# Optimization experiments

Hardware: AMD Instinct MI355X
Metric: run time of the kernel (lower is better)

The kernel has to match this reference:

```python
import jax, jax.numpy as jnp
import numpy as np

B, IN, OUT, BR = 64, 8192, 2048, 4
VTH = 0.5
_SQRT_2PI = float(np.sqrt(2.0 * np.pi))


def _gauss(x, mu, sigma):
    return jnp.exp(-((x - mu) ** 2) / (2.0 * sigma ** 2)) / _SQRT_2PI / sigma


@jax.custom_vjp
def act_fun(x):
    return (x > 0.0).astype(x.dtype)


def _act_fwd(x):
    return act_fun(x), x


def _act_bwd(x, g):
    lens, scale, hight, gamma = 0.5, 6.0, 0.15, 0.5
    temp = (_gauss(x, 0.0, lens) * (1.0 + hight)
            - _gauss(x, lens, scale * lens) * hight
            - _gauss(x, -lens, scale * lens) * hight)
    return (g * temp * gamma,)


act_fun.defvjp(_act_fwd, _act_bwd)


def setup_inputs() -> dict:
    key = jax.random.key(0)
    ks = jax.random.split(key, 8)
    fan_in = IN
    bound = 1.0 / np.sqrt(fan_in)
    return {
        "input_spike": jax.random.uniform(ks[0], (B, IN), dtype=jnp.float32),
        "mem": jax.random.uniform(ks[1], (B, OUT), dtype=jnp.float32),
        "spike": jax.random.uniform(ks[2], (B, OUT), dtype=jnp.float32),
        "d_input": jnp.zeros((B, OUT, BR), dtype=jnp.float32),
        "v_th": jnp.ones((B, OUT), dtype=jnp.float32) * VTH,
        "W": jax.random.uniform(ks[3], (OUT * BR, IN), minval=-bound, maxval=bound, dtype=jnp.float32),
        "b": jax.random.uniform(ks[4], (OUT * BR,), minval=-bound, maxval=bound, dtype=jnp.float32),
        "tau_m": jax.random.uniform(ks[5], (OUT,), minval=0.0, maxval=4.0, dtype=jnp.float32),
        "tau_n": jax.random.uniform(ks[6], (OUT, BR), minval=0.0, maxval=4.0, dtype=jnp.float32),
    }


def reference(input_spike, mem, spike, d_input, v_th, W, b, tau_m, tau_n):
    R_m = 1.0
    batch = input_spike.shape[0]
    out_dim, branch = tau_n.shape
    in_dim = W.shape[1]  # padded input size
    chunk = in_dim // branch
    # pad input to in_dim (pad == 0 for these dims, kept for generality)
    pad = in_dim - input_spike.shape[1]
    k = jnp.pad(input_spike.astype(jnp.float32), ((0, 0), (0, pad)))
    # block-masked linear: mask keeps, for neuron o / branch j, only column block j.
    # Equivalent to taking the diagonal blocks of W reshaped [out, branch, branch, chunk].
    W_diag = jnp.einsum("obbc->obc", W.reshape(out_dim, branch, branch, chunk))
    y = jnp.einsum("obc,nbc->nob", W_diag, k.reshape(batch, branch, chunk))
    y = y + b.reshape(out_dim, branch)  # [B, out, branch]
    # per-branch dendritic decay
    beta = jax.nn.sigmoid(tau_n)
    d_new = beta * d_input + (1.0 - beta) * y
    l_input = d_new.sum(axis=2)  # [B, out]
    # LIF with soft reset
    alpha = jax.nn.sigmoid(tau_m)
    mem_new = mem * alpha + (1.0 - alpha) * R_m * l_input - v_th * spike
    spike_new = act_fun(mem_new - v_th)
    return mem_new, spike_new
```

## Files before the change

kernel.cpp:

```cpp
#include <hip/hip_runtime.h>
#include <math.h>

#define BATCH   64
#define IN_DIM  8192
#define OUT_DIM 2048
#define BRANCH  4
#define CHUNK   2048
#define NSEG    2
#define KSEG    1024
#define KT      128
#define NT      8

typedef __attribute__((ext_vector_type(8))) short short8;
typedef __attribute__((ext_vector_type(4))) short short4v;
typedef __attribute__((ext_vector_type(4))) float f32x4;

__device__ __forceinline__ float sigmoidf_(float x) {
    return 1.0f / (1.0f + expf(-x));
}

__device__ __forceinline__ unsigned rne_bf16(float f) {
    unsigned u = __float_as_uint(f);
    return (u + 0x7fffu + ((u >> 16) & 1u)) >> 16;
}

#define LBAR()                                                   \
    do {                                                         \
        asm volatile("s_waitcnt lgkmcnt(0)" ::: "memory");       \
        __builtin_amdgcn_s_barrier();                            \
        asm volatile("" ::: "memory");                           \
    } while (0)

__global__ __launch_bounds__(256) void prep_x(const float* __restrict__ X,
                                              short8* __restrict__ Xfh,
                                              short8* __restrict__ Xfl) {
    const int gid = blockIdx.x * 256 + threadIdx.x;
    const int l  = gid & 63;
    const int kk = (gid >> 6) & 63;
    const int s  = (gid >> 12) & 3;
    const int j  = gid >> 14;
    const int n  = s * 16 + (l & 15);
    const int k0 = kk * 32 + ((l >> 4) << 3);
    const float* p = X + (size_t)n * IN_DIM + j * CHUNK + k0;
    const f32x4 a = *(const f32x4*)p;
    const f32x4 c = *(const f32x4*)(p + 4);
    float v[8] = {a[0], a[1], a[2], a[3], c[0], c[1], c[2], c[3]};
    short8 h, lo;
#pragma unroll
    for (int e = 0; e < 8; ++e) {
        unsigned hb = rne_bf16(v[e]);
        float fh = __uint_as_float(hb << 16);
        unsigned lb = rne_bf16(v[e] - fh);
        h[e]  = (short)hb;
        lo[e] = (short)lb;
    }
    Xfh[gid] = h;
    Xfl[gid] = lo;
}

__device__ __forceinline__ void stage_store(char* Wh, char* Wl, const f32x4* wr,
                                            int wbyte0, int swz, int kq) {
#pragma unroll
    for (int i = 0; i < 4; ++i) {
        unsigned hb[4], lb[4];
#pragma unroll
        for (int e = 0; e < 4; ++e) {
            float f = wr[i][e];
            unsigned h = rne_bf16(f);
            float fh = __uint_as_float(h << 16);
            unsigned l = rne_bf16(f - fh);
            hb[e] = h; lb[e] = l;
        }
        short4v vh = { (short)hb[0], (short)hb[1], (short)hb[2], (short)hb[3] };
        short4v vl = { (short)lb[0], (short)lb[1], (short)lb[2], (short)lb[3] };
        const int kb   = (kq << 5) + (i << 3);
        const int byte = wbyte0 + (kb ^ swz);
        *(short4v*)(Wh + byte) = vh;
        *(short4v*)(Wl + byte) = vl;
    }
}

__global__ __launch_bounds__(256) void dend_gemm(const short8* __restrict__ Xfh,
                                                 const short8* __restrict__ Xfl,
                                                 const float*  __restrict__ W,
                                                 float* __restrict__ Yp) {
    __shared__ __align__(16) char WhL[2][32 * 256];
    __shared__ __align__(16) char WlL[2][32 * 256];
    __shared__ float Ys[32][65];

    const int t    = threadIdx.x;
    const int bid  = blockIdx.x;
    const int j    = bid & 3;
    const int o0   = ((bid >> 2) & 63) << 5;
    const int ks   = bid >> 8;
    const int lane = t & 63;
    const int wv   = t >> 6;

    const int ri  = t >> 3;
    const int kq  = t & 7;
    const float* wsrc = W + (size_t)((o0 + ri) * 4 + j) * IN_DIM
                          + j * CHUNK + ks * KSEG + kq * 16;
    const int wbyte0 = ri << 8;
    const int swz    = (ri & 15) << 4;

    const short8* pAh = Xfh + (j * 4 + wv) * 4096 + ks * 2048 + lane;
    const short8* pAl = Xfl + (j * 4 + wv) * 4096 + ks * 2048 + lane;

    const int o_l   = lane & 15;
    const int bswz  = o_l << 4;
    const int kgrp  = (lane >> 4) << 4;
    const int b0row = o_l << 8;
    const int b1row = (o_l + 16) << 8;

    f32x4 acc0 = {0.f, 0.f, 0.f, 0.f};
    f32x4 acc1 = {0.f, 0.f, 0.f, 0.f};

    f32x4  wr[4];
    short8 Ah0[4], Al0[4], Ah1[4], Al1[4];

#pragma unroll
    for (int i = 0; i < 4; ++i)
        wr[i] = *(const f32x4*)(wsrc + i * 4);
    stage_store(WhL[0], WlL[0], wr, wbyte0, swz, kq);
#pragma unroll
    for (int i = 0; i < 4; ++i)
        wr[i] = *(const f32x4*)(wsrc + KT + i * 4);
#pragma unroll
    for (int i = 0; i < 4; ++i) { Ah0[i] = pAh[i * 64];       Al0[i] = pAl[i * 64]; }
#pragma unroll
    for (int i = 0; i < 4; ++i) { Ah1[i] = pAh[(4 + i) * 64]; Al1[i] = pAl[(4 + i) * 64]; }
    LBAR();

#define BODY(kt, AH, AL)                                                            \
  {                                                                                 \
    if ((kt) + 1 < NT)                                                              \
        stage_store(WhL[((kt) + 1) & 1], WlL[((kt) + 1) & 1], wr, wbyte0, swz, kq); \
    if ((kt) + 2 < NT) {                                                            \
        _Pragma("unroll")                                                           \
        for (int i = 0; i < 4; ++i)                                                 \
            wr[i] = *(const f32x4*)(wsrc + ((kt) + 2) * KT + i * 4);                \
    }                                                                               \
    _Pragma("unroll")                                                               \
    for (int st = 0; st < 4; ++st) {                                                \
        const int off = ((st << 6) + kgrp) ^ bswz;                                  \
        short8 bh0 = *(const short8*)(&WhL[(kt) & 1][b0row + off]);                 \
        short8 bl0 = *(const short8*)(&WlL[(kt) & 1][b0row + off]);                 \
        short8 bh1 = *(const short8*)(&WhL[(kt) & 1][b1row + off]);                 \
        short8 bl1 = *(const short8*)(&WlL[(kt) & 1][b1row + off]);                 \
        acc0 = __builtin_amdgcn_mfma_f32_16x16x32_bf16(AH[st], bh0, acc0, 0, 0, 0); \
        acc1 = __builtin_amdgcn_mfma_f32_16x16x32_bf16(AH[st], bh1, acc1, 0, 0, 0); \
        acc0 = __builtin_amdgcn_mfma_f32_16x16x32_bf16(AL[st], bh0, acc0, 0, 0, 0); \
        acc1 = __builtin_amdgcn_mfma_f32_16x16x32_bf16(AL[st], bh1, acc1, 0, 0, 0); \
        acc0 = __builtin_amdgcn_mfma_f32_16x16x32_bf16(AH[st], bl0, acc0, 0, 0, 0); \
        acc1 = __builtin_amdgcn_mfma_f32_16x16x32_bf16(AH[st], bl1, acc1, 0, 0, 0); \
    }                                                                               \
    if ((kt) + 2 < NT) {                                                            \
        _Pragma("unroll")                                                           \
        for (int i = 0; i < 4; ++i) {                                               \
            AH[i] = pAh[(((kt) + 2) * 4 + i) * 64];                                 \
            AL[i] = pAl[(((kt) + 2) * 4 + i) * 64];                                 \
        }                                                                           \
    }                                                                               \
    LBAR();                                                                         \
  }

#pragma unroll 1
    for (int kt = 0; kt < NT; kt += 2) {
        BODY(kt,     Ah0, Al0)
        BODY(kt + 1, Ah1, Al1)
    }
#undef BODY

    {
        const int rb = (wv << 4) + ((lane >> 4) << 2);
#pragma unroll
        for (int r = 0; r < 4; ++r) {
            Ys[o_l][rb + r]      = acc0[r];
            Ys[o_l + 16][rb + r] = acc1[r];
        }
    }
    __syncthreads();
#pragma unroll
    for (int p = 0; p < 8; ++p) {
        const int e  = t + (p << 8);
        const int oo = e & 31;
        const int n  = e >> 5;
        Yp[(size_t)(((ks * BATCH + n) << 2) + j) * OUT_DIM + o0 + oo] = Ys[oo][n];
    }
}

__global__ __launch_bounds__(256) void lif_pointwise(
    const float* __restrict__ Yp,
    const float* __restrict__ mem,
    const float* __restrict__ spike,
    const float* __restrict__ d_input,
    const float* __restrict__ v_th,
    const float* __restrict__ b,
    const float* __restrict__ tau_m,
    const float* __restrict__ tau_n,
    float* __restrict__ out)
{
    const int idx = blockIdx.x * 256 + threadIdx.x;
    const int o   = idx & (OUT_DIM - 1);
    const int n   = idx >> 11;

    const float4 tn = ((const float4*)tau_n)[o];
    const float4 bb = ((const float4*)b)[o];
    const float4 di = ((const float4*)d_input)[idx];

    float y0 = 0.f, y1 = 0.f, y2 = 0.f, y3 = 0.f;
#pragma unroll
    for (int s = 0; s < NSEG; ++s) {
        const size_t base = (size_t)((s * BATCH + n) << 2) * OUT_DIM + o;
        y0 += Yp[base];
        y1 += Yp[base + OUT_DIM];
        y2 += Yp[base + 2 * OUT_DIM];
        y3 += Yp[base + 3 * OUT_DIM];
    }

    float l = 0.0f;
    { const float bt = sigmoidf_(tn.x); l += bt * di.x + (1.0f - bt) * (y0 + bb.x); }
    { const float bt = sigmoidf_(tn.y); l += bt * di.y + (1.0f - bt) * (y1 + bb.y); }
    { const float bt = sigmoidf_(tn.z); l += bt * di.z + (1.0f - bt) * (y2 + bb.z); }
    { const float bt = sigmoidf_(tn.w); l += bt * di.w + (1.0f - bt) * (y3 + bb.w); }

    const float alpha = sigmoidf_(tau_m[o]);
    const float vt    = v_th[idx];
    const float m     = mem[idx] * alpha + (1.0f - alpha) * l - vt * spike[idx];

    out[idx] = m;
    out[BATCH * OUT_DIM + idx] = (m - vt) > 0.0f ? 1.0f : 0.0f;
}

extern "C" void kernel_launch(void* const* d_in, const int* in_sizes, int n_in,
                              void* d_out, int out_size, void* d_ws, size_t ws_size,
                              hipStream_t stream) {
    const float* X     = (const float*)d_in[0];
    const float* mem   = (const float*)d_in[1];
    const float* spike = (const float*)d_in[2];
    const float* dinp  = (const float*)d_in[3];
    const float* vth   = (const float*)d_in[4];
    const float* W     = (const float*)d_in[5];
    const float* b     = (const float*)d_in[6];
    const float* tm    = (const float*)d_in[7];
    const float* tn    = (const float*)d_in[8];
    float* out = (float*)d_out;

    short8* Xfh = (short8*)d_ws;
    short8* Xfl = (short8*)((char*)d_ws + (1u << 20));
    float*  Yp  = (float*)((char*)d_ws + (2u << 20));

    prep_x<<<256, 256, 0, stream>>>(X, Xfh, Xfl);
    dend_gemm<<<512, 256, 0, stream>>>(Xfh, Xfl, W, Yp);
    lif_pointwise<<<512, 256, 0, stream>>>(Yp, mem, spike, dinp, vth, b, tm, tn, out);
}
```

Measured before the change: 28.01 us.

## Fuse X bf16 hi/lo split into GEMM and use truncation instead of RNE

```diff
diff --git a/kernel.cpp b/kernel.cpp
--- a/kernel.cpp
+++ b/kernel.cpp
@@ -19,11 +19,6 @@
     return 1.0f / (1.0f + expf(-x));
 }
 
-__device__ __forceinline__ unsigned rne_bf16(float f) {
-    unsigned u = __float_as_uint(f);
-    return (u + 0x7fffu + ((u >> 16) & 1u)) >> 16;
-}
-
 #define LBAR()                                                   \
     do {                                                         \
         asm volatile("s_waitcnt lgkmcnt(0)" ::: "memory");       \
@@ -31,31 +26,17 @@
         asm volatile("" ::: "memory");                           \
     } while (0)
 
-__global__ __launch_bounds__(256) void prep_x(const float* __restrict__ X,
-                                              short8* __restrict__ Xfh,
-                                              short8* __restrict__ Xfl) {
-    const int gid = blockIdx.x * 256 + threadIdx.x;
-    const int l  = gid & 63;
-    const int kk = (gid >> 6) & 63;
-    const int s  = (gid >> 12) & 3;
-    const int j  = gid >> 14;
-    const int n  = s * 16 + (l & 15);
-    const int k0 = kk * 32 + ((l >> 4) << 3);
-    const float* p = X + (size_t)n * IN_DIM + j * CHUNK + k0;
-    const f32x4 a = *(const f32x4*)p;
-    const f32x4 c = *(const f32x4*)(p + 4);
-    float v[8] = {a[0], a[1], a[2], a[3], c[0], c[1], c[2], c[3]};
-    short8 h, lo;
+__device__ __forceinline__ void tsplit8(const f32x4 a, const f32x4 b,
+                                        short8& h, short8& lo) {
 #pragma unroll
     for (int e = 0; e < 8; ++e) {
-        unsigned hb = rne_bf16(v[e]);
-        float fh = __uint_as_float(hb << 16);
-        unsigned lb = rne_bf16(v[e] - fh);
-        h[e]  = (short)hb;
-        lo[e] = (short)lb;
-    }
-    Xfh[gid] = h;
-    Xfl[gid] = lo;
+        const float f  = (e < 4) ? a[e] : b[e - 4];
+        const unsigned u  = __float_as_uint(f);
+        const unsigned hu = u & 0xffff0000u;
+        const float fl = f - __uint_as_float(hu);
+        h[e]  = (short)(u >> 16);
+        lo[e] = (short)(__float_as_uint(fl) >> 16);
+    }
 }
 
 __device__ __forceinline__ void stage_store(char* Wh, char* Wl, const f32x4* wr,
@@ -65,11 +46,12 @@
         unsigned hb[4], lb[4];
 #pragma unroll
         for (int e = 0; e < 4; ++e) {
-            float f = wr[i][e];
-            unsigned h = rne_bf16(f);
-            float fh = __uint_as_float(h << 16);
-            unsigned l = rne_bf16(f - fh);
-            hb[e] = h; lb[e] = l;
+            const float f  = wr[i][e];
+            const unsigned u  = __float_as_uint(f);
+            const unsigned hu = u & 0xffff0000u;
+            const float fl = f - __uint_as_float(hu);
+            hb[e] = u >> 16;
+            lb[e] = __float_as_uint(fl) >> 16;
         }
         short4v vh = { (short)hb[0], (short)hb[1], (short)hb[2], (short)hb[3] };
         short4v vl = { (short)lb[0], (short)lb[1], (short)lb[2], (short)lb[3] };
@@ -80,8 +62,7 @@
     }
 }
 
-__global__ __launch_bounds__(256) void dend_gemm(const short8* __restrict__ Xfh,
-                                                 const short8* __restrict__ Xfl,
+__global__ __launch_bounds__(256) void dend_gemm(const float* __restrict__ X,
                                                  const float*  __restrict__ W,
                                                  float* __restrict__ Yp) {
     __shared__ __align__(16) char WhL[2][32 * 256];
@@ -103,14 +84,15 @@
     const int wbyte0 = ri << 8;
     const int swz    = (ri & 15) << 4;
 
-    const short8* pAh = Xfh + (j * 4 + wv) * 4096 + ks * 2048 + lane;
-    const short8* pAl = Xfl + (j * 4 + wv) * 4096 + ks * 2048 + lane;
-
     const int o_l   = lane & 15;
+    const int q     = lane >> 4;
     const int bswz  = o_l << 4;
-    const int kgrp  = (lane >> 4) << 4;
+    const int kgrp  = q << 4;
     const int b0row = o_l << 8;
     const int b1row = (o_l + 16) << 8;
+
+    const float* xsrc = X + (size_t)(wv * 16 + o_l) * IN_DIM
+                          + j * CHUNK + ks * KSEG + q * 8;
 
     f32x4 acc0 = {0.f, 0.f, 0.f, 0.f};
     f32x4 acc1 = {0.f, 0.f, 0.f, 0.f};
@@ -126,9 +108,15 @@
     for (int i = 0; i < 4; ++i)
         wr[i] = *(const f32x4*)(wsrc + KT + i * 4);
 #pragma unroll
-    for (int i = 0; i < 4; ++i) { Ah0[i] = pAh[i * 64];       Al0[i] = pAl[i * 64]; }
-#pragma unroll
-    for (int i = 0; i < 4; ++i) { Ah1[i] = pAh[(4 + i) * 64]; Al1[i] = pAl[(4 + i) * 64]; }
+    for (int i = 0; i < 4; ++i) {
+        const float* xp = xsrc + i * 32;
+        tsplit8(*(const f32x4*)xp, *(const f32x4*)(xp + 4), Ah0[i], Al0[i]);
+    }
+#pragma unroll
+    for (int i = 0; i < 4; ++i) {
+        const float* xp = xsrc + (4 + i) * 32;
+        tsplit8(*(const f32x4*)xp, *(const f32x4*)(xp + 4), Ah1[i], Al1[i]);
+    }
     LBAR();
 
 #define BODY(kt, AH, AL)                                                            \
@@ -139,6 +127,15 @@
         _Pragma("unroll")                                                           \
         for (int i = 0; i < 4; ++i)                                                 \
             wr[i] = *(const f32x4*)(wsrc + ((kt) + 2) * KT + i * 4);                \
+    }                                                                               \
+    f32x4 xa[4], xc[4];                                                             \
+    if ((kt) + 2 < NT) {                                                            \
+        _Pragma("unroll")                                                           \
+        for (int i = 0; i < 4; ++i) {                                               \
+            const float* xp = xsrc + (((kt) + 2) * 4 + i) * 32;                     \
+            xa[i] = *(const f32x4*)xp;                                              \
+            xc[i] = *(const f32x4*)(xp + 4);                                        \
+        }                                                                           \
     }                                                                               \
     _Pragma("unroll")                                                               \
     for (int st = 0; st < 4; ++st) {                                                \
@@ -156,10 +153,8 @@
     }                                                                               \
     if ((kt) + 2 < NT) {                                                            \
         _Pragma("unroll")                                                           \
-        for (int i = 0; i < 4; ++i) {                                               \
-            AH[i] = pAh[(((kt) + 2) * 4 + i) * 64];                                 \
-            AL[i] = pAl[(((kt) + 2) * 4 + i) * 64];                                 \
-        }                                                                           \
+        for (int i = 0; i < 4; ++i)                                                 \
+            tsplit8(xa[i], xc[i], AH[i], AL[i]);                                    \
     }                                                                               \
     LBAR();                                                                         \
   }
@@ -172,7 +167,7 @@
 #undef BODY
 
     {
-        const int rb = (wv << 4) + ((lane >> 4) << 2);
+        const int rb = (wv << 4) + (q << 2);
 #pragma unroll
         for (int r = 0; r < 4; ++r) {
             Ys[o_l][rb + r]      = acc0[r];
@@ -246,11 +241,8 @@
     const float* tn    = (const float*)d_in[8];
     float* out = (float*)d_out;
 
-    short8* Xfh = (short8*)d_ws;
-    short8* Xfl = (short8*)((char*)d_ws + (1u << 20));
-    float*  Yp  = (float*)((char*)d_ws + (2u << 20));
-
-    prep_x<<<256, 256, 0, stream>>>(X, Xfh, Xfl);
-    dend_gemm<<<512, 256, 0, stream>>>(Xfh, Xfl, W, Yp);
+    float* Yp = (float*)d_ws;
+
+    dend_gemm<<<512, 256, 0, stream>>>(X, W, Yp);
     lif_pointwise<<<512, 256, 0, stream>>>(Yp, mem, spike, dinp, vth, b, tm, tn, out);
 }
```

Result: slower. 30.19 us (+7.8%).

## Fuse dendritic GEMM with LIF pointwise epilogue, drop split-K partials

Applied to the files above, without the earlier changes.

```diff
diff --git a/kernel.cpp b/kernel.cpp
--- a/kernel.cpp
+++ b/kernel.cpp
@@ -6,10 +6,8 @@
 #define OUT_DIM 2048
 #define BRANCH  4
 #define CHUNK   2048
-#define NSEG    2
-#define KSEG    1024
 #define KT      128
-#define NT      8
+#define NTILE   16
 
 typedef __attribute__((ext_vector_type(8))) short short8;
 typedef __attribute__((ext_vector_type(4))) short short4v;
@@ -80,156 +78,150 @@
     }
 }
 
-__global__ __launch_bounds__(256) void dend_gemm(const short8* __restrict__ Xfh,
-                                                 const short8* __restrict__ Xfl,
-                                                 const float*  __restrict__ W,
-                                                 float* __restrict__ Yp) {
-    __shared__ __align__(16) char WhL[2][32 * 256];
-    __shared__ __align__(16) char WlL[2][32 * 256];
-    __shared__ float Ys[32][65];
+__global__ __launch_bounds__(512) void dend_fused(
+    const short8* __restrict__ Xfh,
+    const short8* __restrict__ Xfl,
+    const float*  __restrict__ W,
+    const float*  __restrict__ mem,
+    const float*  __restrict__ spike,
+    const float*  __restrict__ d_input,
+    const float*  __restrict__ v_th,
+    const float*  __restrict__ bias,
+    const float*  __restrict__ tau_m,
+    const float*  __restrict__ tau_n,
+    float* __restrict__ out)
+{
+    __shared__ __align__(16) char WhL[2][64 * 256];
+    __shared__ __align__(16) char WlL[2][64 * 256];
 
     const int t    = threadIdx.x;
     const int bid  = blockIdx.x;
-    const int j    = bid & 3;
-    const int o0   = ((bid >> 2) & 63) << 5;
-    const int ks   = bid >> 8;
     const int lane = t & 63;
     const int wv   = t >> 6;
+    const int nsp  = wv >> 2;
+    const int j    = wv & 3;
 
     const int ri  = t >> 3;
     const int kq  = t & 7;
-    const float* wsrc = W + (size_t)((o0 + ri) * 4 + j) * IN_DIM
-                          + j * CHUNK + ks * KSEG + kq * 16;
+    const float* wsrc = W + (size_t)(bid * 64 + ri) * IN_DIM
+                          + (ri & 3) * CHUNK + kq * 16;
     const int wbyte0 = ri << 8;
-    const int swz    = (ri & 15) << 4;
-
-    const short8* pAh = Xfh + (j * 4 + wv) * 4096 + ks * 2048 + lane;
-    const short8* pAl = Xfl + (j * 4 + wv) * 4096 + ks * 2048 + lane;
-
-    const int o_l   = lane & 15;
-    const int bswz  = o_l << 4;
-    const int kgrp  = (lane >> 4) << 4;
-    const int b0row = o_l << 8;
-    const int b1row = (o_l + 16) << 8;
+    const int swz    = ((ri >> 2) & 15) << 4;
+
+    const int o_l  = lane & 15;
+    const int q    = lane >> 4;
+    const int brow = (o_l * 4 + j) << 8;
+    const int bswz = o_l << 4;
+    const int kgrp = q << 4;
+
+    const int s0 = nsp * 2;
+    const short8* pAh0 = Xfh + (j * 4 + s0) * 4096 + lane;
+    const short8* pAl0 = Xfl + (j * 4 + s0) * 4096 + lane;
+    const short8* pAh1 = pAh0 + 4096;
+    const short8* pAl1 = pAl0 + 4096;
 
     f32x4 acc0 = {0.f, 0.f, 0.f, 0.f};
     f32x4 acc1 = {0.f, 0.f, 0.f, 0.f};
 
     f32x4  wr[4];
-    short8 Ah0[4], Al0[4], Ah1[4], Al1[4];
+    short8 AXh0[2], AXl0[2], AXh1[2], AXl1[2];
+    short8 AYh0[2], AYl0[2], AYh1[2], AYl1[2];
+
+#define LOADA(P, base)                                         \
+  if ((base) < 64) {                                           \
+    _Pragma("unroll")                                          \
+    for (int u = 0; u < 2; ++u) {                              \
+        A##P##h0[u] = pAh0[((base) + u) * 64];                 \
+        A##P##l0[u] = pAl0[((base) + u) * 64];                 \
+        A##P##h1[u] = pAh1[((base) + u) * 64];                 \
+        A##P##l1[u] = pAl1[((base) + u) * 64];                 \
+    }                                                          \
+  }
+
+#define CONSUME(P, kt, stbase)                                                        \
+  { _Pragma("unroll")                                                                 \
+    for (int u = 0; u < 2; ++u) {                                                     \
+        const int off = ((((stbase) + u) << 6) + kgrp) ^ bswz;                        \
+        const short8 bh = *(const short8*)(&WhL[(kt) & 1][brow + off]);               \
+        const short8 bl = *(const short8*)(&WlL[(kt) & 1][brow + off]);               \
+        acc0 = __builtin_amdgcn_mfma_f32_16x16x32_bf16(A##P##h0[u], bh, acc0, 0,0,0); \
+        acc1 = __builtin_amdgcn_mfma_f32_16x16x32_bf16(A##P##h1[u], bh, acc1, 0,0,0); \
+        acc0 = __builtin_amdgcn_mfma_f32_16x16x32_bf16(A##P##l0[u], bh, acc0, 0,0,0); \
+        acc1 = __builtin_amdgcn_mfma_f32_16x16x32_bf16(A##P##l1[u], bh, acc1, 0,0,0); \
+        acc0 = __builtin_amdgcn_mfma_f32_16x16x32_bf16(A##P##h0[u], bl, acc0, 0,0,0); \
+        acc1 = __builtin_amdgcn_mfma_f32_16x16x32_bf16(A##P##h1[u], bl, acc1, 0,0,0); \
+    } }
 
 #pragma unroll
     for (int i = 0; i < 4; ++i)
         wr[i] = *(const f32x4*)(wsrc + i * 4);
-    stage_store(WhL[0], WlL[0], wr, wbyte0, swz, kq);
+    stage_store(&WhL[0][0], &WlL[0][0], wr, wbyte0, swz, kq);
 #pragma unroll
     for (int i = 0; i < 4; ++i)
         wr[i] = *(const f32x4*)(wsrc + KT + i * 4);
-#pragma unroll
-    for (int i = 0; i < 4; ++i) { Ah0[i] = pAh[i * 64];       Al0[i] = pAl[i * 64]; }
-#pragma unroll
-    for (int i = 0; i < 4; ++i) { Ah1[i] = pAh[(4 + i) * 64]; Al1[i] = pAl[(4 + i) * 64]; }
+    LOADA(X, 0)
     LBAR();
 
-#define BODY(kt, AH, AL)                                                            \
-  {                                                                                 \
-    if ((kt) + 1 < NT)                                                              \
-        stage_store(WhL[((kt) + 1) & 1], WlL[((kt) + 1) & 1], wr, wbyte0, swz, kq); \
-    if ((kt) + 2 < NT) {                                                            \
-        _Pragma("unroll")                                                           \
-        for (int i = 0; i < 4; ++i)                                                 \
-            wr[i] = *(const f32x4*)(wsrc + ((kt) + 2) * KT + i * 4);                \
-    }                                                                               \
-    _Pragma("unroll")                                                               \
-    for (int st = 0; st < 4; ++st) {                                                \
-        const int off = ((st << 6) + kgrp) ^ bswz;                                  \
-        short8 bh0 = *(const short8*)(&WhL[(kt) & 1][b0row + off]);                 \
-        short8 bl0 = *(const short8*)(&WlL[(kt) & 1][b0row + off]);                 \
-        short8 bh1 = *(const short8*)(&WhL[(kt) & 1][b1row + off]);                 \
-        short8 bl1 = *(const short8*)(&WlL[(kt) & 1][b1row + off]);                 \
-        acc0 = __builtin_amdgcn_mfma_f32_16x16x32_bf16(AH[st], bh0, acc0, 0, 0, 0); \
-        acc1 = __builtin_amdgcn_mfma_f32_16x16x32_bf16(AH[st], bh1, acc1, 0, 0, 0); \
-        acc0 = __builtin_amdgcn_mfma_f32_16x16x32_bf16(AL[st], bh0, acc0, 0, 0, 0); \
-        acc1 = __builtin_amdgcn_mfma_f32_16x16x32_bf16(AL[st], bh1, acc1, 0, 0, 0); \
-        acc0 = __builtin_amdgcn_mfma_f32_16x16x32_bf16(AH[st], bl0, acc0, 0, 0, 0); \
-        acc1 = __builtin_amdgcn_mfma_f32_16x16x32_bf16(AH[st], bl1, acc1, 0, 0, 0); \
-    }                                                                               \
-    if ((kt) + 2 < NT) {                                                            \
-        _Pragma("unroll")                                                           \
-        for (int i = 0; i < 4; ++i) {                                               \
-            AH[i] = pAh[(((kt) + 2) * 4 + i) * 64];                                 \
-            AL[i] = pAl[(((kt) + 2) * 4 + i) * 64];                                 \
-        }                                                                           \
-    }                                                                               \
-    LBAR();                                                                         \
-  }
-
 #pragma unroll 1
-    for (int kt = 0; kt < NT; kt += 2) {
-        BODY(kt,     Ah0, Al0)
-        BODY(kt + 1, Ah1, Al1)
-    }
-#undef BODY
-
+    for (int kt = 0; kt < NTILE; ++kt) {
+        if (kt + 1 < NTILE)
+            stage_store(&WhL[(kt + 1) & 1][0], &WlL[(kt + 1) & 1][0],
+                        wr, wbyte0, swz, kq);
+        if (kt + 2 < NTILE) {
+#pragma unroll
+            for (int i = 0; i < 4; ++i)
+                wr[i] = *(const f32x4*)(wsrc + (kt + 2) * KT + i * 4);
+        }
+        LOADA(Y, kt * 4 + 2)
+        CONSUME(X, kt, 0)
+        LOADA(X, kt * 4 + 4)
+        CONSUME(Y, kt, 2)
+        LBAR();
+    }
+#undef LOADA
+#undef CONSUME
+
+    float* Ysum = (float*)&WhL[0][0];
     {
-        const int rb = (wv << 4) + ((lane >> 4) << 2);
 #pragma unroll
         for (int r = 0; r < 4; ++r) {
-            Ys[o_l][rb + r]      = acc0[r];
-            Ys[o_l + 16][rb + r] = acc1[r];
+            const int n0 = s0 * 16 + q * 4 + r;
+            Ysum[(j * 64 + n0)      * 17 + o_l] = acc0[r];
+            Ysum[(j * 64 + n0 + 16) * 17 + o_l] = acc1[r];
         }
     }
     __syncthreads();
-#pragma unroll
-    for (int p = 0; p < 8; ++p) {
-        const int e  = t + (p << 8);
-        const int oo = e & 31;
-        const int n  = e >> 5;
-        Yp[(size_t)(((ks * BATCH + n) << 2) + j) * OUT_DIM + o0 + oo] = Ys[oo][n];
-    }
-}
-
-__global__ __launch_bounds__(256) void lif_pointwise(
-    const float* __restrict__ Yp,
-    const float* __restrict__ mem,
-    const float* __restrict__ spike,
-    const float* __restrict__ d_input,
-    const float* __restrict__ v_th,
-    const float* __restrict__ b,
-    const float* __restrict__ tau_m,
-    const float* __restrict__ tau_n,
-    float* __restrict__ out)
-{
-    const int idx = blockIdx.x * 256 + threadIdx.x;
-    const int o   = idx & (OUT_DIM - 1);
-    const int n   = idx >> 11;
-
-    const float4 tn = ((const float4*)tau_n)[o];
-    const float4 bb = ((const float4*)b)[o];
-    const float4 di = ((const float4*)d_input)[idx];
-
-    float y0 = 0.f, y1 = 0.f, y2 = 0.f, y3 = 0.f;
-#pragma unroll
-    for (int s = 0; s < NSEG; ++s) {
-        const size_t base = (size_t)((s * BATCH + n) << 2) * OUT_DIM + o;
-        y0 += Yp[base];
-        y1 += Yp[base + OUT_DIM];
-        y2 += Yp[base + 2 * OUT_DIM];
-        y3 += Yp[base + 3 * OUT_DIM];
-    }
-
-    float l = 0.0f;
-    { const float bt = sigmoidf_(tn.x); l += bt * di.x + (1.0f - bt) * (y0 + bb.x); }
-    { const float bt = sigmoidf_(tn.y); l += bt * di.y + (1.0f - bt) * (y1 + bb.y); }
-    { const float bt = sigmoidf_(tn.z); l += bt * di.z + (1.0f - bt) * (y2 + bb.z); }
-    { const float bt = sigmoidf_(tn.w); l += bt * di.w + (1.0f - bt) * (y3 + bb.w); }
-
-    const float alpha = sigmoidf_(tau_m[o]);
-    const float vt    = v_th[idx];
-    const float m     = mem[idx] * alpha + (1.0f - alpha) * l - vt * spike[idx];
-
-    out[idx] = m;
-    out[BATCH * OUT_DIM + idx] = (m - vt) > 0.0f ? 1.0f : 0.0f;
+
+#pragma unroll
+    for (int p = 0; p < 2; ++p) {
+        const int e  = t + p * 512;
+        const int oo = e & 15;
+        const int n  = e >> 4;
+        const int og = bid * 16 + oo;
+        const int idx = n * OUT_DIM + og;
+
+        const float y0 = Ysum[(0 * 64 + n) * 17 + oo];
+        const float y1 = Ysum[(1 * 64 + n) * 17 + oo];
+        const float y2 = Ysum[(2 * 64 + n) * 17 + oo];
+        const float y3 = Ysum[(3 * 64 + n) * 17 + oo];
+
+        const float4 tn = ((const float4*)tau_n)[og];
+        const float4 bb = ((const float4*)bias)[og];
+        const float4 di = ((const float4*)d_input)[idx];
+
+        float l = 0.0f;
+        { const float bt = sigmoidf_(tn.x); l += bt * di.x + (1.0f - bt) * (y0 + bb.x); }
+        { const float bt = sigmoidf_(tn.y); l += bt * di.y + (1.0f - bt) * (y1 + bb.y); }
+        { const float bt = sigmoidf_(tn.z); l += bt * di.z + (1.0f - bt) * (y2 + bb.z); }
+        { const float bt = sigmoidf_(tn.w); l += bt * di.w + (1.0f - bt) * (y3 + bb.w); }
+
+        const float alpha = sigmoidf_(tau_m[og]);
+        const float vt    = v_th[idx];
+        const float m     = mem[idx] * alpha + (1.0f - alpha) * l - vt * spike[idx];
+
+        out[idx] = m;
+        out[BATCH * OUT_DIM + idx] = (m - vt) > 0.0f ? 1.0f : 0.0f;
+    }
 }
 
 extern "C" void kernel_launch(void* const* d_in, const int* in_sizes, int n_in,
@@ -248,9 +240,8 @@
 
     short8* Xfh = (short8*)d_ws;
     short8* Xfl = (short8*)((char*)d_ws + (1u << 20));
-    float*  Yp  = (float*)((char*)d_ws + (2u << 20));
 
     prep_x<<<256, 256, 0, stream>>>(X, Xfh, Xfl);
-    dend_gemm<<<512, 256, 0, stream>>>(Xfh, Xfl, W, Yp);
-    lif_pointwise<<<512, 256, 0, stream>>>(Yp, mem, spike, dinp, vth, b, tm, tn, out);
-}
+    dend_fused<<<128, 512, 0, stream>>>(Xfh, Xfl, W, mem, spike, dinp, vth,
+                                        b, tm, tn, out);
+}
```

After: 47.22 us. +68.6%, slower.
